# Optimization experiments

Measured on AMD Instinct MI355X. Metric: run time of the kernel, lower is better.

## Reference

```python
import jax, jax.numpy as jnp
import numpy as np

EPS = 1e-8
LAMBDA_SOFTMAX = 9.0
LAMBDA_LSE = 6.0
LEAKY = 0.1


def _l2norm(x, axis):
    n = jnp.sqrt(jnp.sum(x * x, axis=axis, keepdims=True)) + EPS
    return x / n


def setup_inputs() -> dict:
    key = jax.random.key(0)
    k1, k2, k3, k4 = jax.random.split(key, 4)
    n_img, n_cap, n_region, max_w, img_dim, d = 64, 64, 36, 32, 2048, 1024
    images = jax.random.normal(k1, (n_img, n_region, img_dim), dtype=jnp.float32)
    cap_emb = jax.random.normal(k2, (n_cap, max_w, d), dtype=jnp.float32)
    # Xavier-uniform fc like EncoderImagePrecomp.init_weights
    r = np.sqrt(6.0) / np.sqrt(img_dim + d)
    W_fc = jax.random.uniform(k3, (img_dim, d), dtype=jnp.float32, minval=-r, maxval=r)
    b_fc = jnp.zeros((d,), dtype=jnp.float32)
    cap_lens = jnp.maximum(jax.random.randint(k4, (n_cap,), 0, max_w), 4).astype(jnp.int32)
    return {"images": images, "cap_emb": cap_emb, "W_fc": W_fc, "b_fc": b_fc, "cap_lens": cap_lens}


def reference(images, cap_emb, W_fc, b_fc, cap_lens):
    # EncoderImagePrecomp: linear projection + l2norm over feature dim
    img_emb = _l2norm(images @ W_fc + b_fc, axis=-1)          # (I, R, d)
    # text_norm (EncoderText applies l2norm to cap_emb)
    cap = _l2norm(cap_emb, axis=-1)                           # (C, W, d)

    C, W = cap.shape[0], cap.shape[1]
    mask = (jnp.arange(W)[None, :] < cap_lens[:, None]).astype(cap.dtype)  # (C, W)

    # func_attention (t2i): query=caption words, context=image regions
    # attn = bmm(context, query^T): (C, I, R, W)
    attn = jnp.einsum('ird,cwd->cirw', img_emb, cap)
    # clipped_l2norm: LeakyReLU(0.1) then l2norm over the word (queryL) axis,
    # with padded words zeroed so the norm matches the ragged per-caption slice
    attn = jnp.where(attn > 0, attn, LEAKY * attn)
    attn = attn * mask[:, None, None, :]
    attn = _l2norm(attn, axis=-1)
    # transpose -> (C, I, W, R), temperature softmax over regions
    attn = jnp.swapaxes(attn, 2, 3)
    attn = jax.nn.softmax(attn * LAMBDA_SOFTMAX, axis=-1)     # (C, I, W, R)
    # weightedContext = attn @ images: (C, I, W, d)
    wctx = jnp.einsum('ciwr,ird->ciwd', attn, img_emb)

    # cosine similarity between caption words and weighted context
    w12 = jnp.einsum('cwd,ciwd->ciw', cap, wctx)
    w1 = jnp.sqrt(jnp.sum(cap * cap, axis=-1))[:, None, :]     # (C, 1, W)
    w2 = jnp.sqrt(jnp.sum(wctx * wctx, axis=-1))               # (C, I, W)
    row_sim = w12 / jnp.maximum(w1 * w2, EPS)                  # (C, I, W)

    # LogSumExp aggregation over valid words only
    e = jnp.exp(row_sim * LAMBDA_LSE) * mask[:, None, :]
    sim = jnp.log(jnp.sum(e, axis=-1)) / LAMBDA_LSE            # (C, I)
    # torch code concatenates per-caption columns -> (n_image, n_caption)
    return sim.T
```

## Files before the change

kernel.cpp:

```cpp
#include <hip/hip_runtime.h>

constexpr int NI = 64;
constexpr int NC = 64;
constexpr int RR = 36;
constexpr int WW = 32;
constexpr int DI = 2048;
constexpr int DD = 1024;
constexpr int MROWS = NI * RR;
constexpr int NCOLS = NC * WW;

#define EPSV 1e-8f
#define LAM_SM 9.0f
#define LAM_LSE 6.0f
#define LEAKY_S 0.1f

typedef __bf16 bf16x8 __attribute__((ext_vector_type(8)));
typedef float f32x4 __attribute__((ext_vector_type(4)));
typedef unsigned short ushort8v __attribute__((ext_vector_type(8)));
typedef unsigned short ushort4v __attribute__((ext_vector_type(4)));

__device__ __forceinline__ unsigned short f2bf(float f) {
    unsigned int u = __builtin_bit_cast(unsigned int, f);
    unsigned int r = (u + 0x7fffu + ((u >> 16) & 1u)) >> 16;
    return (unsigned short)r;
}

#define GLOAD16(gp, lp)                                                              \
    __builtin_amdgcn_global_load_lds(                                                \
        (const __attribute__((address_space(1))) unsigned int*)(gp),                 \
        (__attribute__((address_space(3))) unsigned int*)(lp), 16, 0, 0)

__global__ __launch_bounds__(256) void prep(const float* __restrict__ images,
                                            const float* __restrict__ W,
                                            const float* __restrict__ cap,
                                            unsigned short* __restrict__ images_bf,
                                            unsigned short* __restrict__ Wt,
                                            unsigned short* __restrict__ capn_bf,
                                            float* __restrict__ w1)
{
    const int b = blockIdx.x, tid = threadIdx.x;
    if (b < 2304) {
        int i = b * 256 + tid;
        const float4* X4 = reinterpret_cast<const float4*>(images);
        float4 a = X4[i * 2], c = X4[i * 2 + 1];
        ushort8v o;
        o[0] = f2bf(a.x); o[1] = f2bf(a.y); o[2] = f2bf(a.z); o[3] = f2bf(a.w);
        o[4] = f2bf(c.x); o[5] = f2bf(c.y); o[6] = f2bf(c.z); o[7] = f2bf(c.w);
        *reinterpret_cast<ushort8v*>(&images_bf[i * 8]) = o;
    } else if (b < 4352) {
        __shared__ float t[32][33];
        int bi = b - 2304;
        int bk = (bi >> 5) * 32;
        int bn = (bi & 31) * 32;
        int x = tid & 31, y0 = tid >> 5;
        for (int yy = y0; yy < 32; yy += 8)
            t[yy][x] = W[(bk + yy) * DD + bn + x];
        __syncthreads();
        for (int yy = y0; yy < 32; yy += 8)
            Wt[(bn + yy) * DI + bk + x] = f2bf(t[x][yy]);
    } else {
        int row = b - 4352;
        float4 v = *reinterpret_cast<const float4*>(&cap[row * 1024 + tid * 4]);
        float s = v.x * v.x + v.y * v.y + v.z * v.z + v.w * v.w;
        #pragma unroll
        for (int off = 32; off; off >>= 1) s += __shfl_down(s, off);
        __shared__ float ps[4];
        if ((tid & 63) == 0) ps[tid >> 6] = s;
        __syncthreads();
        float tot = ps[0] + ps[1] + ps[2] + ps[3];
        float n = sqrtf(tot);
        float inv = 1.0f / (n + EPSV);
        v.x *= inv; v.y *= inv; v.z *= inv; v.w *= inv;
        ushort4v o;
        o[0] = f2bf(v.x); o[1] = f2bf(v.y); o[2] = f2bf(v.z); o[3] = f2bf(v.w);
        *reinterpret_cast<ushort4v*>(&capn_bf[row * 1024 + tid * 4]) = o;
        if (tid == 0) w1[row] = n * inv;
    }
}

template <int M, int N, int K, int KS>
__global__ __launch_bounds__(256) void gemm_proj64(const unsigned short* __restrict__ A,
                                                   const unsigned short* __restrict__ Bt,
                                                   float* __restrict__ C)
{
    __shared__ __align__(16) unsigned short As[64 * 64];
    __shared__ __align__(16) unsigned short Bs[128 * 64];
    const int tid = threadIdx.x;
    const int w = tid >> 6, lane = tid & 63;
    const int bm = blockIdx.x * 64, bn = blockIdx.y * 128;
    const int klo = blockIdx.z * (K / KS);
    const int wr = w >> 1, wc = w & 1;
    const int hi = lane >> 4, fr = lane & 15;

    f32x4 acc[2][4] = {};

    const unsigned short* gA[2];
    const unsigned short* gB[4];
    unsigned short* lA[2];
    unsigned short* lB[4];
    #pragma unroll
    for (int n = 0; n < 2; ++n) {
        int s = tid + n * 256;
        int row = s >> 3, j = (s & 7) ^ (row & 7);
        gA[n] = &A[(size_t)(bm + row) * K + klo + j * 8];
        lA[n] = &As[s * 8];
    }
    #pragma unroll
    for (int n = 0; n < 4; ++n) {
        int s = tid + n * 256;
        int row = s >> 3, j = (s & 7) ^ (row & 7);
        gB[n] = &Bt[(size_t)(bn + row) * K + klo + j * 8];
        lB[n] = &Bs[s * 8];
    }

    for (int k0 = 0; k0 < K / KS; k0 += 64) {
        __syncthreads();
        #pragma unroll
        for (int n = 0; n < 2; ++n) GLOAD16(gA[n] + k0, lA[n]);
        #pragma unroll
        for (int n = 0; n < 4; ++n) GLOAD16(gB[n] + k0, lB[n]);
        __syncthreads();
        #pragma unroll
        for (int ks = 0; ks < 2; ++ks) {
            bf16x8 af[2], bfv[4];
            #pragma unroll
            for (int mi = 0; mi < 2; ++mi) {
                int row = wr * 32 + mi * 16 + fr;
                af[mi] = *reinterpret_cast<const bf16x8*>(
                    &As[row * 64 + ((((ks << 2) + hi) ^ (row & 7)) << 3)]);
            }
            #pragma unroll
            for (int ni = 0; ni < 4; ++ni) {
                int row = wc * 64 + ni * 16 + fr;
                bfv[ni] = *reinterpret_cast<const bf16x8*>(
                    &Bs[row * 64 + ((((ks << 2) + hi) ^ (row & 7)) << 3)]);
            }
            #pragma unroll
            for (int mi = 0; mi < 2; ++mi)
                #pragma unroll
                for (int ni = 0; ni < 4; ++ni)
                    acc[mi][ni] = __builtin_amdgcn_mfma_f32_16x16x32_bf16(af[mi], bfv[ni], acc[mi][ni], 0, 0, 0);
        }
    }

    float* Cz = C + (size_t)blockIdx.z * M * N;
    const int cr0 = hi * 4, cc = fr;
    #pragma unroll
    for (int mi = 0; mi < 2; ++mi) {
        int row0 = bm + wr * 32 + mi * 16 + cr0;
        #pragma unroll
        for (int ni = 0; ni < 4; ++ni) {
            int col = bn + wc * 64 + ni * 16 + cc;
            #pragma unroll
            for (int r = 0; r < 4; ++r)
                Cz[(size_t)(row0 + r) * N + col] = acc[mi][ni][r];
        }
    }
}

__global__ __launch_bounds__(256) void rownorm_add(const float* __restrict__ P0,
                                                   const float* __restrict__ P1,
                                                   const float* __restrict__ bias,
                                                   unsigned short* __restrict__ Xbf)
{
    const int row = blockIdx.x;
    const int t4 = threadIdx.x * 4;
    float4 a = *reinterpret_cast<const float4*>(&P0[row * 1024 + t4]);
    float4 b = *reinterpret_cast<const float4*>(&P1[row * 1024 + t4]);
    float4 c = *reinterpret_cast<const float4*>(&bias[t4]);
    float4 v = {a.x + b.x + c.x, a.y + b.y + c.y, a.z + b.z + c.z, a.w + b.w + c.w};
    float s = v.x * v.x + v.y * v.y + v.z * v.z + v.w * v.w;
    #pragma unroll
    for (int off = 32; off; off >>= 1) s += __shfl_down(s, off);
    __shared__ float ps[4];
    if ((threadIdx.x & 63) == 0) ps[threadIdx.x >> 6] = s;
    __syncthreads();
    float tot = ps[0] + ps[1] + ps[2] + ps[3];
    float inv = 1.0f / (sqrtf(tot) + EPSV);
    v.x *= inv; v.y *= inv; v.z *= inv; v.w *= inv;
    ushort4v o;
    o[0] = f2bf(v.x); o[1] = f2bf(v.y); o[2] = f2bf(v.z); o[3] = f2bf(v.w);
    *reinterpret_cast<ushort4v*>(&Xbf[row * 1024 + t4]) = o;
}

__global__ __launch_bounds__(256) void sim_fused(const unsigned short* __restrict__ img_bf,
                                                 const unsigned short* __restrict__ capn_bf,
                                                 const float* __restrict__ w1v,
                                                 const int* __restrict__ cap_lens,
                                                 float* __restrict__ out)
{
    __shared__ __align__(16) unsigned short As[48 * 32];
    __shared__ __align__(16) unsigned short Bs[128 * 32];
    __shared__ __align__(16) unsigned short Gb[48 * 64];
    __shared__ __align__(16) unsigned short Eb[4][32 * 64];
    const int tid = threadIdx.x;
    const int w = tid >> 6, lane = tid & 63;
    const int i = blockIdx.y, cg = blockIdx.x;
    const int c = cg * 4 + w;
    const int hi = lane >> 4, lo = lane & 15;

    {
        unsigned int* gdst = (unsigned int*)Gb;
        for (int e = tid; e < 48 * 8; e += 256)
            gdst[(e >> 3) * 32 + 24 + (e & 7)] = 0;
        unsigned int* ed = (unsigned int*)Eb;
        for (int e2 = tid; e2 < 4 * 32 * 8; e2 += 256) {
            int slab = e2 >> 8, rem = e2 & 255;
            ed[slab * 1024 + (rem >> 3) * 32 + 24 + (rem & 7)] = 0;
        }
    }

    f32x4 acc[3][2] = {};
    f32x4 gacc0 = {0.f, 0.f, 0.f, 0.f}, gacc1 = {0.f, 0.f, 0.f, 0.f}, gacc2 = {0.f, 0.f, 0.f, 0.f};
    const unsigned short* gA0 = &img_bf[(size_t)(i * RR + (tid >> 2)) * DD + (tid & 3) * 8];
    const unsigned short* gB0 = &capn_bf[(size_t)(cg * 128 + (tid >> 2)) * DD + (tid & 3) * 8];
    unsigned short* lA0 = &As[w * 512];
    unsigned short* lB0 = &Bs[w * 512];
    const int kgrp = hi * 8;

    for (int k0 = 0; k0 < DD; k0 += 32) {
        __syncthreads();
        if (w < 3) GLOAD16(gA0 + k0, lA0);
        GLOAD16(gB0 + k0, lB0);
        GLOAD16(gB0 + 64 * DD + k0, lB0 + 2048);
        __syncthreads();
        bf16x8 b0 = *reinterpret_cast<const bf16x8*>(&Bs[(w * 32 + lo) * 32 + kgrp]);
        bf16x8 b1 = *reinterpret_cast<const bf16x8*>(&Bs[(w * 32 + 16 + lo) * 32 + kgrp]);
        bf16x8 af0 = *reinterpret_cast<const bf16x8*>(&As[(0 * 16 + lo) * 32 + kgrp]);
        bf16x8 af1 = *reinterpret_cast<const bf16x8*>(&As[(1 * 16 + lo) * 32 + kgrp]);
        bf16x8 af2 = *reinterpret_cast<const bf16x8*>(&As[(2 * 16 + lo) * 32 + kgrp]);
        acc[0][0] = __builtin_amdgcn_mfma_f32_16x16x32_bf16(af0, b0, acc[0][0], 0, 0, 0);
        acc[0][1] = __builtin_amdgcn_mfma_f32_16x16x32_bf16(af0, b1, acc[0][1], 0, 0, 0);
        acc[1][0] = __builtin_amdgcn_mfma_f32_16x16x32_bf16(af1, b0, acc[1][0], 0, 0, 0);
        acc[1][1] = __builtin_amdgcn_mfma_f32_16x16x32_bf16(af1, b1, acc[1][1], 0, 0, 0);
        acc[2][0] = __builtin_amdgcn_mfma_f32_16x16x32_bf16(af2, b0, acc[2][0], 0, 0, 0);
        acc[2][1] = __builtin_amdgcn_mfma_f32_16x16x32_bf16(af2, b1, acc[2][1], 0, 0, 0);
        if (w == 0) {
            gacc0 = __builtin_amdgcn_mfma_f32_16x16x32_bf16(af0, af0, gacc0, 0, 0, 0);
            gacc1 = __builtin_amdgcn_mfma_f32_16x16x32_bf16(af0, af1, gacc1, 0, 0, 0);
            gacc2 = __builtin_amdgcn_mfma_f32_16x16x32_bf16(af0, af2, gacc2, 0, 0, 0);
        } else if (w == 1) {
            gacc0 = __builtin_amdgcn_mfma_f32_16x16x32_bf16(af1, af0, gacc0, 0, 0, 0);
            gacc1 = __builtin_amdgcn_mfma_f32_16x16x32_bf16(af1, af1, gacc1, 0, 0, 0);
            gacc2 = __builtin_amdgcn_mfma_f32_16x16x32_bf16(af1, af2, gacc2, 0, 0, 0);
        } else if (w == 2) {
            gacc0 = __builtin_amdgcn_mfma_f32_16x16x32_bf16(af2, af0, gacc0, 0, 0, 0);
            gacc1 = __builtin_amdgcn_mfma_f32_16x16x32_bf16(af2, af1, gacc1, 0, 0, 0);
            gacc2 = __builtin_amdgcn_mfma_f32_16x16x32_bf16(af2, af2, gacc2, 0, 0, 0);
        }
    }

    if (w < 3) {
        #pragma unroll
        for (int reg = 0; reg < 4; ++reg) {
            int grow = (w * 16 + hi * 4 + reg) * 64;
            Gb[grow + 0 * 16 + lo] = f2bf(gacc0[reg]);
            Gb[grow + 1 * 16 + lo] = f2bf(gacc1[reg]);
            Gb[grow + 2 * 16 + lo] = f2bf(gacc2[reg]);
        }
    }

    const int len = cap_lens[c];

    float a1[3][2][4];
    #pragma unroll
    for (int mi = 0; mi < 3; ++mi)
        #pragma unroll
        for (int reg = 0; reg < 4; ++reg) {
            int r = mi * 16 + hi * 4 + reg;
            float v0 = acc[mi][0][reg]; v0 = v0 > 0.f ? v0 : LEAKY_S * v0; v0 = (lo < len) ? v0 : 0.f;
            float v1 = acc[mi][1][reg]; v1 = v1 > 0.f ? v1 : LEAKY_S * v1; v1 = (16 + lo < len) ? v1 : 0.f;
            float ss = v0 * v0 + v1 * v1;
            ss += __shfl_xor(ss, 1); ss += __shfl_xor(ss, 2);
            ss += __shfl_xor(ss, 4); ss += __shfl_xor(ss, 8);
            float inv = 1.0f / (sqrtf(ss) + EPSV);
            bool valid = r < RR;
            a1[mi][0][reg] = valid ? v0 * inv : -1e30f;
            a1[mi][1][reg] = valid ? v1 * inv : -1e30f;
        }

    float m0 = -1e30f, m1 = -1e30f;
    #pragma unroll
    for (int mi = 0; mi < 3; ++mi)
        #pragma unroll
        for (int reg = 0; reg < 4; ++reg) {
            m0 = fmaxf(m0, a1[mi][0][reg]);
            m1 = fmaxf(m1, a1[mi][1][reg]);
        }
    m0 = fmaxf(m0, __shfl_xor(m0, 16)); m0 = fmaxf(m0, __shfl_xor(m0, 32));
    m1 = fmaxf(m1, __shfl_xor(m1, 16)); m1 = fmaxf(m1, __shfl_xor(m1, 32));

    float e_[3][2][4];
    float w12p0 = 0.f, w12p1 = 0.f;
    #pragma unroll
    for (int mi = 0; mi < 3; ++mi)
        #pragma unroll
        for (int reg = 0; reg < 4; ++reg) {
            int r = mi * 16 + hi * 4 + reg;
            bool valid = r < RR;
            float e0 = valid ? __expf(LAM_SM * (a1[mi][0][reg] - m0)) : 0.f;
            float e1 = valid ? __expf(LAM_SM * (a1[mi][1][reg] - m1)) : 0.f;
            e_[mi][0][reg] = e0; e_[mi][1][reg] = e1;
            w12p0 += e0 * acc[mi][0][reg];
            w12p1 += e1 * acc[mi][1][reg];
            Eb[w][(lo) * 64 + r] = f2bf(e0);
            Eb[w][(16 + lo) * 64 + r] = f2bf(e1);
        }
    w12p0 += __shfl_xor(w12p0, 16); w12p0 += __shfl_xor(w12p0, 32);
    w12p1 += __shfl_xor(w12p1, 16); w12p1 += __shfl_xor(w12p1, 32);
    __syncthreads();

    f32x4 T[3][2] = {};
    #pragma unroll
    for (int kk = 0; kk < 2; ++kk) {
        int kg2 = kk * 32 + hi * 8;
        bf16x8 eb0 = *reinterpret_cast<const bf16x8*>(&Eb[w][(lo) * 64 + kg2]);
        bf16x8 eb1 = *reinterpret_cast<const bf16x8*>(&Eb[w][(16 + lo) * 64 + kg2]);
        #pragma unroll
        for (int mi = 0; mi < 3; ++mi) {
            bf16x8 gf = *reinterpret_cast<const bf16x8*>(&Gb[(mi * 16 + lo) * 64 + kg2]);
            T[mi][0] = __builtin_amdgcn_mfma_f32_16x16x32_bf16(gf, eb0, T[mi][0], 0, 0, 0);
            T[mi][1] = __builtin_amdgcn_mfma_f32_16x16x32_bf16(gf, eb1, T[mi][1], 0, 0, 0);
        }
    }
    float w20 = 0.f, w21 = 0.f;
    #pragma unroll
    for (int mi = 0; mi < 3; ++mi)
        #pragma unroll
        for (int reg = 0; reg < 4; ++reg) {
            w20 += e_[mi][0][reg] * T[mi][0][reg];
            w21 += e_[mi][1][reg] * T[mi][1][reg];
        }
    w20 += __shfl_xor(w20, 16); w20 += __shfl_xor(w20, 32);
    w21 += __shfl_xor(w21, 16); w21 += __shfl_xor(w21, 32);

    float ew = 0.f;
    if (lo < len) {
        float rs = w12p0 / fmaxf(w1v[c * WW + lo] * sqrtf(fmaxf(w20, 0.f)), 1e-30f);
        ew += __expf(LAM_LSE * rs);
    }
    if (16 + lo < len) {
        float rs = w12p1 / fmaxf(w1v[c * WW + 16 + lo] * sqrtf(fmaxf(w21, 0.f)), 1e-30f);
        ew += __expf(LAM_LSE * rs);
    }
    ew += __shfl_xor(ew, 1); ew += __shfl_xor(ew, 2);
    ew += __shfl_xor(ew, 4); ew += __shfl_xor(ew, 8);
    if (lane == 0) out[i * NC + c] = logf(ew) / LAM_LSE;
}

extern "C" void kernel_launch(void* const* d_in, const int* in_sizes, int n_in,
                              void* d_out, int out_size, void* d_ws, size_t ws_size,
                              hipStream_t stream)
{
    const float* images   = (const float*)d_in[0];
    const float* cap_emb  = (const float*)d_in[1];
    const float* W_fc     = (const float*)d_in[2];
    const float* b_fc     = (const float*)d_in[3];
    const int*   cap_lens = (const int*)d_in[4];
    float* out = (float*)d_out;

    char* ws = (char*)d_ws;
    float*          part0     = (float*)(ws);
    float*          part1     = (float*)(ws + 9437184);
    unsigned short* images_bf = (unsigned short*)(ws + 18874368);
    unsigned short* Wt        = (unsigned short*)(ws + 28311552);
    unsigned short* img_bf    = (unsigned short*)(ws + 32505856);
    unsigned short* capn_bf   = (unsigned short*)(ws + 37224448);
    float*          w1        = (float*)(ws + 41713664);

    prep<<<6400, 256, 0, stream>>>(images, W_fc, cap_emb, images_bf, Wt, capn_bf, w1);
    gemm_proj64<MROWS, DD, DI, 2><<<dim3(MROWS / 64, DD / 128, 2), 256, 0, stream>>>(images_bf, Wt, part0);
    rownorm_add<<<MROWS, 256, 0, stream>>>(part0, part1, b_fc, img_bf);
    sim_fused<<<dim3(16, NI), 256, 0, stream>>>(img_bf, capn_bf, w1, cap_lens, out);
}
```

Measured before the change: 150.6 us.

## Double K-tile depth to 64, XOR-swizzle LDS tiles, pad Gram/E buffers

The main GEMM loop now stages 64 K-elements per iteration instead of 32, which halves the number of barrier pairs and global-to-LDS load rounds. The A and B tiles are stored in LDS with an XOR swizzle on 16-byte chunks so that MFMA operand reads avoid bank conflicts. The Gram and softmax-weight buffers move from a row stride of 64 to 72 elements for the same reason. LDS use rises, which may lower occupancy, and each thread now issues more load instructions per stage.

```diff
diff --git a/kernel.cpp b/kernel.cpp
--- a/kernel.cpp
+++ b/kernel.cpp
@@ -189,10 +189,10 @@
                                                  const int* __restrict__ cap_lens,
                                                  float* __restrict__ out)
 {
-    __shared__ __align__(16) unsigned short As[48 * 32];
-    __shared__ __align__(16) unsigned short Bs[128 * 32];
-    __shared__ __align__(16) unsigned short Gb[48 * 64];
-    __shared__ __align__(16) unsigned short Eb[4][32 * 64];
+    __shared__ __align__(16) unsigned short As[48 * 64];
+    __shared__ __align__(16) unsigned short Bs[128 * 64];
+    __shared__ __align__(16) unsigned short Gb[48 * 72];
+    __shared__ __align__(16) unsigned short Eb[4][32 * 72];
     const int tid = threadIdx.x;
     const int w = tid >> 6, lane = tid & 63;
     const int i = blockIdx.y, cg = blockIdx.x;
@@ -202,58 +202,76 @@
     {
         unsigned int* gdst = (unsigned int*)Gb;
         for (int e = tid; e < 48 * 8; e += 256)
-            gdst[(e >> 3) * 32 + 24 + (e & 7)] = 0;
+            gdst[(e >> 3) * 36 + 24 + (e & 7)] = 0;
         unsigned int* ed = (unsigned int*)Eb;
         for (int e2 = tid; e2 < 4 * 32 * 8; e2 += 256) {
             int slab = e2 >> 8, rem = e2 & 255;
-            ed[slab * 1024 + (rem >> 3) * 32 + 24 + (rem & 7)] = 0;
-        }
+            ed[slab * 1152 + (rem >> 3) * 36 + 24 + (rem & 7)] = 0;
+        }
+    }
+
+    const unsigned short* gAs[2];
+    unsigned short* lAs[2];
+    #pragma unroll
+    for (int n = 0; n < 2; ++n) {
+        int s = w * 128 + n * 64 + lane;
+        int row = s >> 3, j = (s & 7) ^ (row & 7);
+        gAs[n] = &img_bf[(size_t)(i * RR + row) * DD + j * 8];
+        lAs[n] = &As[s * 8];
+    }
+    const unsigned short* gBs[4];
+    unsigned short* lBs[4];
+    #pragma unroll
+    for (int n = 0; n < 4; ++n) {
+        int s = w * 256 + n * 64 + lane;
+        int row = s >> 3, j = (s & 7) ^ (row & 7);
+        gBs[n] = &capn_bf[(size_t)(cg * 128 + row) * DD + j * 8];
+        lBs[n] = &Bs[s * 8];
     }
 
     f32x4 acc[3][2] = {};
     f32x4 gacc0 = {0.f, 0.f, 0.f, 0.f}, gacc1 = {0.f, 0.f, 0.f, 0.f}, gacc2 = {0.f, 0.f, 0.f, 0.f};
-    const unsigned short* gA0 = &img_bf[(size_t)(i * RR + (tid >> 2)) * DD + (tid & 3) * 8];
-    const unsigned short* gB0 = &capn_bf[(size_t)(cg * 128 + (tid >> 2)) * DD + (tid & 3) * 8];
-    unsigned short* lA0 = &As[w * 512];
-    unsigned short* lB0 = &Bs[w * 512];
-    const int kgrp = hi * 8;
-
-    for (int k0 = 0; k0 < DD; k0 += 32) {
-        __syncthreads();
-        if (w < 3) GLOAD16(gA0 + k0, lA0);
-        GLOAD16(gB0 + k0, lB0);
-        GLOAD16(gB0 + 64 * DD + k0, lB0 + 2048);
-        __syncthreads();
-        bf16x8 b0 = *reinterpret_cast<const bf16x8*>(&Bs[(w * 32 + lo) * 32 + kgrp]);
-        bf16x8 b1 = *reinterpret_cast<const bf16x8*>(&Bs[(w * 32 + 16 + lo) * 32 + kgrp]);
-        bf16x8 af0 = *reinterpret_cast<const bf16x8*>(&As[(0 * 16 + lo) * 32 + kgrp]);
-        bf16x8 af1 = *reinterpret_cast<const bf16x8*>(&As[(1 * 16 + lo) * 32 + kgrp]);
-        bf16x8 af2 = *reinterpret_cast<const bf16x8*>(&As[(2 * 16 + lo) * 32 + kgrp]);
-        acc[0][0] = __builtin_amdgcn_mfma_f32_16x16x32_bf16(af0, b0, acc[0][0], 0, 0, 0);
-        acc[0][1] = __builtin_amdgcn_mfma_f32_16x16x32_bf16(af0, b1, acc[0][1], 0, 0, 0);
-        acc[1][0] = __builtin_amdgcn_mfma_f32_16x16x32_bf16(af1, b0, acc[1][0], 0, 0, 0);
-        acc[1][1] = __builtin_amdgcn_mfma_f32_16x16x32_bf16(af1, b1, acc[1][1], 0, 0, 0);
-        acc[2][0] = __builtin_amdgcn_mfma_f32_16x16x32_bf16(af2, b0, acc[2][0], 0, 0, 0);
-        acc[2][1] = __builtin_amdgcn_mfma_f32_16x16x32_bf16(af2, b1, acc[2][1], 0, 0, 0);
-        if (w == 0) {
-            gacc0 = __builtin_amdgcn_mfma_f32_16x16x32_bf16(af0, af0, gacc0, 0, 0, 0);
-            gacc1 = __builtin_amdgcn_mfma_f32_16x16x32_bf16(af0, af1, gacc1, 0, 0, 0);
-            gacc2 = __builtin_amdgcn_mfma_f32_16x16x32_bf16(af0, af2, gacc2, 0, 0, 0);
-        } else if (w == 1) {
-            gacc0 = __builtin_amdgcn_mfma_f32_16x16x32_bf16(af1, af0, gacc0, 0, 0, 0);
-            gacc1 = __builtin_amdgcn_mfma_f32_16x16x32_bf16(af1, af1, gacc1, 0, 0, 0);
-            gacc2 = __builtin_amdgcn_mfma_f32_16x16x32_bf16(af1, af2, gacc2, 0, 0, 0);
-        } else if (w == 2) {
-            gacc0 = __builtin_amdgcn_mfma_f32_16x16x32_bf16(af2, af0, gacc0, 0, 0, 0);
-            gacc1 = __builtin_amdgcn_mfma_f32_16x16x32_bf16(af2, af1, gacc1, 0, 0, 0);
-            gacc2 = __builtin_amdgcn_mfma_f32_16x16x32_bf16(af2, af2, gacc2, 0, 0, 0);
+
+    for (int k0 = 0; k0 < DD; k0 += 64) {
+        __syncthreads();
+        if (w < 3) { GLOAD16(gAs[0] + k0, lAs[0]); GLOAD16(gAs[1] + k0, lAs[1]); }
+        GLOAD16(gBs[0] + k0, lBs[0]); GLOAD16(gBs[1] + k0, lBs[1]);
+        GLOAD16(gBs[2] + k0, lBs[2]); GLOAD16(gBs[3] + k0, lBs[3]);
+        __syncthreads();
+        #pragma unroll
+        for (int ks = 0; ks < 2; ++ks) {
+            const int co = ((((ks << 2) + hi) ^ (lo & 7)) << 3);
+            bf16x8 b0  = *reinterpret_cast<const bf16x8*>(&Bs[(w * 32 + lo) * 64 + co]);
+            bf16x8 b1  = *reinterpret_cast<const bf16x8*>(&Bs[(w * 32 + 16 + lo) * 64 + co]);
+            bf16x8 af0 = *reinterpret_cast<const bf16x8*>(&As[(lo) * 64 + co]);
+            bf16x8 af1 = *reinterpret_cast<const bf16x8*>(&As[(16 + lo) * 64 + co]);
+            bf16x8 af2 = *reinterpret_cast<const bf16x8*>(&As[(32 + lo) * 64 + co]);
+            acc[0][0] = __builtin_amdgcn_mfma_f32_16x16x32_bf16(af0, b0, acc[0][0], 0, 0, 0);
+            acc[0][1] = __builtin_amdgcn_mfma_f32_16x16x32_bf16(af0, b1, acc[0][1], 0, 0, 0);
+            acc[1][0] = __builtin_amdgcn_mfma_f32_16x16x32_bf16(af1, b0, acc[1][0], 0, 0, 0);
+            acc[1][1] = __builtin_amdgcn_mfma_f32_16x16x32_bf16(af1, b1, acc[1][1], 0, 0, 0);
+            acc[2][0] = __builtin_amdgcn_mfma_f32_16x16x32_bf16(af2, b0, acc[2][0], 0, 0, 0);
+            acc[2][1] = __builtin_amdgcn_mfma_f32_16x16x32_bf16(af2, b1, acc[2][1], 0, 0, 0);
+            if (w == 0) {
+                gacc0 = __builtin_amdgcn_mfma_f32_16x16x32_bf16(af0, af0, gacc0, 0, 0, 0);
+                gacc1 = __builtin_amdgcn_mfma_f32_16x16x32_bf16(af0, af1, gacc1, 0, 0, 0);
+                gacc2 = __builtin_amdgcn_mfma_f32_16x16x32_bf16(af0, af2, gacc2, 0, 0, 0);
+            } else if (w == 1) {
+                gacc0 = __builtin_amdgcn_mfma_f32_16x16x32_bf16(af1, af0, gacc0, 0, 0, 0);
+                gacc1 = __builtin_amdgcn_mfma_f32_16x16x32_bf16(af1, af1, gacc1, 0, 0, 0);
+                gacc2 = __builtin_amdgcn_mfma_f32_16x16x32_bf16(af1, af2, gacc2, 0, 0, 0);
+            } else if (w == 2) {
+                gacc0 = __builtin_amdgcn_mfma_f32_16x16x32_bf16(af2, af0, gacc0, 0, 0, 0);
+                gacc1 = __builtin_amdgcn_mfma_f32_16x16x32_bf16(af2, af1, gacc1, 0, 0, 0);
+                gacc2 = __builtin_amdgcn_mfma_f32_16x16x32_bf16(af2, af2, gacc2, 0, 0, 0);
+            }
         }
     }
 
     if (w < 3) {
         #pragma unroll
         for (int reg = 0; reg < 4; ++reg) {
-            int grow = (w * 16 + hi * 4 + reg) * 64;
+            int grow = (w * 16 + hi * 4 + reg) * 72;
             Gb[grow + 0 * 16 + lo] = f2bf(gacc0[reg]);
             Gb[grow + 1 * 16 + lo] = f2bf(gacc1[reg]);
             Gb[grow + 2 * 16 + lo] = f2bf(gacc2[reg]);
@@ -303,8 +321,8 @@
             e_[mi][0][reg] = e0; e_[mi][1][reg] = e1;
             w12p0 += e0 * acc[mi][0][reg];
             w12p1 += e1 * acc[mi][1][reg];
-            Eb[w][(lo) * 64 + r] = f2bf(e0);
-            Eb[w][(16 + lo) * 64 + r] = f2bf(e1);
+            Eb[w][(lo) * 72 + r] = f2bf(e0);
+            Eb[w][(16 + lo) * 72 + r] = f2bf(e1);
         }
     w12p0 += __shfl_xor(w12p0, 16); w12p0 += __shfl_xor(w12p0, 32);
     w12p1 += __shfl_xor(w12p1, 16); w12p1 += __shfl_xor(w12p1, 32);
@@ -314,11 +332,11 @@
     #pragma unroll
     for (int kk = 0; kk < 2; ++kk) {
         int kg2 = kk * 32 + hi * 8;
-        bf16x8 eb0 = *reinterpret_cast<const bf16x8*>(&Eb[w][(lo) * 64 + kg2]);
-        bf16x8 eb1 = *reinterpret_cast<const bf16x8*>(&Eb[w][(16 + lo) * 64 + kg2]);
+        bf16x8 eb0 = *reinterpret_cast<const bf16x8*>(&Eb[w][(lo) * 72 + kg2]);
+        bf16x8 eb1 = *reinterpret_cast<const bf16x8*>(&Eb[w][(16 + lo) * 72 + kg2]);
         #pragma unroll
         for (int mi = 0; mi < 3; ++mi) {
-            bf16x8 gf = *reinterpret_cast<const bf16x8*>(&Gb[(mi * 16 + lo) * 64 + kg2]);
+            bf16x8 gf = *reinterpret_cast<const bf16x8*>(&Gb[(mi * 16 + lo) * 72 + kg2]);
             T[mi][0] = __builtin_amdgcn_mfma_f32_16x16x32_bf16(gf, eb0, T[mi][0], 0, 0, 0);
             T[mi][1] = __builtin_amdgcn_mfma_f32_16x16x32_bf16(gf, eb1, T[mi][1], 0, 0, 0);
         }
```

After: 145.1 us. 1.04x faster.
